# Kernel optimization log

Hardware: AMD Instinct MI355X
Metric: run time of the kernel (lower is better)

Reference implementation:

```python
import jax, jax.numpy as jnp
import numpy as np

N_USERS = 100000
N_ITEMS = 50000
N_FACTORS = 64
N_LAYERS = 3
NNZ = 4800000


def setup_inputs() -> dict:
    key = jax.random.key(0)
    k1, k2, k3, k4, k5 = jax.random.split(key, 5)
    N = N_USERS + N_ITEMS
    return {
        "user_emb": 0.1 * jax.random.normal(k1, (N_USERS, N_FACTORS), dtype=jnp.float32),
        "item_emb": 0.1 * jax.random.normal(k2, (N_ITEMS, N_FACTORS), dtype=jnp.float32),
        "adj_row": jax.random.randint(k3, (NNZ,), 0, N, dtype=jnp.int32),
        "adj_col": jax.random.randint(k4, (NNZ,), 0, N, dtype=jnp.int32),
        "adj_val": jax.random.uniform(k5, (NNZ,), dtype=jnp.float32),
    }


def reference(user_emb, item_emb, adj_row, adj_col, adj_val):
    n_users = user_emb.shape[0]
    n_items = item_emb.shape[0]
    N = n_users + n_items

    # initial embeddings: concat users then items  [N, d]
    emb = jnp.concatenate([user_emb, item_emb], axis=0)

    def spmm(x):
        # sparse (COO) @ dense: gather source rows, scale, scatter-add to dest rows
        msgs = adj_val[:, None] * x[adj_col]          # [nnz, d]
        return jax.ops.segment_sum(msgs, adj_row, num_segments=N)

    # running mean over layer outputs (fuses stack+mean; dropout=0, eval mode)
    acc = emb
    for _ in range(N_LAYERS):
        emb = spmm(emb)
        acc = acc + emb
    mean_emb = acc / (N_LAYERS + 1)

    return mean_emb[:n_users], mean_emb[n_users:]
```

## Files before the change

kernel.cpp:

```cpp
#include <hip/hip_runtime.h>

static constexpr int D        = 64;
static constexpr int N_LAYERS = 3;
static constexpr int SH2      = 8;
static constexpr int T1       = 4096;
static constexpr int CAP      = 8896;
static constexpr int NINIT    = 448;

__device__ inline unsigned pack_bf2(float a, float b) {
    unsigned ua = __float_as_uint(a); ua = (ua + 0x7FFFu + ((ua >> 16) & 1u)) >> 16;
    unsigned ub = __float_as_uint(b); ub = (ub + 0x7FFFu + ((ub >> 16) & 1u)) >> 16;
    return ua | (ub << 16);
}
__device__ inline float blo(unsigned u) { return __uint_as_float(u << 16); }
__device__ inline float bhi(unsigned u) { return __uint_as_float(u & 0xFFFF0000u); }

__global__ __launch_bounds__(256) void k_part1f(const int* __restrict__ row,
                                                const int* __restrict__ col,
                                                const float* __restrict__ val,
                                                int* __restrict__ gcnt,
                                                int2* __restrict__ gout,
                                                int nnz, int NB2, int nInit,
                                                const float4* __restrict__ ue,
                                                const float4* __restrict__ ie,
                                                uint4* __restrict__ cur,
                                                int nUser8, int nTot8) {
    __shared__ int2 ebuf[T1];
    __shared__ unsigned short bbin[T1];
    __shared__ unsigned short perm[T1];
    __shared__ int hist[768];
    __shared__ int binstart[768];
    __shared__ int gcur[768];
    __shared__ int bincur[768];
    __shared__ int ssum[256];

    int tid = threadIdx.x;
    int bid = blockIdx.x;
    int tile;
    if (bid < 2 * nInit) {
        if (bid & 1) {
            int stride = nInit * 256;
            for (int i = (bid >> 1) * 256 + tid; i < nTot8; i += stride) {
                float4 f0, f1;
                if (i < nUser8) { f0 = ue[2 * i];              f1 = ue[2 * i + 1]; }
                else            { int j = i - nUser8; f0 = ie[2 * j]; f1 = ie[2 * j + 1]; }
                cur[i] = make_uint4(pack_bf2(f0.x, f0.y), pack_bf2(f0.z, f0.w),
                                    pack_bf2(f1.x, f1.y), pack_bf2(f1.z, f1.w));
            }
            return;
        }
        tile = bid >> 1;
    } else {
        tile = bid - nInit;
    }

    int base = tile * T1;
    int n    = nnz - base; if (n > T1) n = T1;

    for (int b = tid; b < NB2; b += 256) { hist[b] = 0; bincur[b] = 0; }
    __syncthreads();

    for (int i = tid; i < n; i += 256) {
        int e = base + i;
        int r = row[e];
        ebuf[i] = make_int2(((r & ((1 << SH2) - 1)) << 18) | col[e],
                            __float_as_int(val[e]));
        int b = r >> SH2;
        bbin[i] = (unsigned short)b;
        atomicAdd(&hist[b], 1);
    }
    __syncthreads();

    int per = (NB2 + 255) / 256;
    int i0  = tid * per;
    int sum = 0;
    for (int k = 0; k < per; ++k) { int i = i0 + k; if (i < NB2) sum += hist[i]; }
    ssum[tid] = sum;
    __syncthreads();
    for (int off = 1; off < 256; off <<= 1) {
        int v = (tid >= off) ? ssum[tid - off] : 0;
        __syncthreads();
        ssum[tid] += v;
        __syncthreads();
    }
    int run = ssum[tid] - sum;
    for (int k = 0; k < per; ++k) {
        int i = i0 + k;
        if (i < NB2) { binstart[i] = run; run += hist[i]; }
    }
    __syncthreads();

    for (int b = tid; b < NB2; b += 256) {
        int c = hist[b];
        if (c) gcur[b] = b * CAP + atomicAdd(&gcnt[b], c);
    }
    __syncthreads();

    for (int i = tid; i < n; i += 256) {
        int b = bbin[i];
        int rnk = binstart[b] + atomicAdd(&bincur[b], 1);
        perm[rnk] = (unsigned short)i;
    }
    __syncthreads();

    for (int j = tid; j < n; j += 256) {
        int i = perm[j];
        int b = bbin[i];
        gout[gcur[b] + (j - binstart[b])] = ebuf[i];
    }
}

__global__ __launch_bounds__(256) void k_part2(const int* __restrict__ gcnt,
                                               int2* __restrict__ gbuf,
                                               int2* __restrict__ rowptr2) {
    __shared__ int2 sbuf[CAP];
    __shared__ int hist[256];
    __shared__ int cur[256];
    __shared__ int ssum[256];
    int b   = blockIdx.x;
    int tid = threadIdx.x;
    int lo  = b * CAP;
    int cnt = gcnt[b];

    hist[tid] = 0;
    __syncthreads();
    for (int i = tid; i < cnt; i += 256) {
        int2 e = gbuf[lo + i];
        sbuf[i] = e;
        atomicAdd(&hist[(unsigned)e.x >> 18], 1);
    }
    __syncthreads();

    int h = hist[tid];
    ssum[tid] = h;
    __syncthreads();
    for (int off = 1; off < 256; off <<= 1) {
        int v = (tid >= off) ? ssum[tid - off] : 0;
        __syncthreads();
        ssum[tid] += v;
        __syncthreads();
    }
    int excl = ssum[tid] - h;
    cur[tid] = excl;
    rowptr2[(b << SH2) + tid] = make_int2(lo + excl, lo + excl + h);
    __syncthreads();

    for (int i = tid; i < cnt; i += 256) {
        int2 e = sbuf[i];
        int r  = (unsigned)e.x >> 18;
        int p  = atomicAdd(&cur[r], 1);
        gbuf[lo + p] = make_int2((e.x & 0x3FFFF) << 3, e.y);
    }
}

template <bool FIRST, bool WRITE_Y, bool LAST>
__global__ void k_spmm_bf(const int2* __restrict__ rowptr2, const int2* __restrict__ ecv,
                          const uint4* __restrict__ x, uint4* __restrict__ y,
                          float* __restrict__ acc,
                          const float* __restrict__ ue, const float* __restrict__ ie,
                          int nUser, int N) {
    int wid = (blockIdx.x * blockDim.x + threadIdx.x) >> 6;
    if (wid >= N) return;
    int lane = threadIdx.x & 63;
    int grp  = lane >> 3;
    int ch   = lane & 7;
    int2 rp = rowptr2[wid];
    int e0 = rp.x;
    int e1 = rp.y;
    float s0 = 0.f, s1 = 0.f, s2 = 0.f, s3 = 0.f;
    float s4 = 0.f, s5 = 0.f, s6 = 0.f, s7 = 0.f;
    int e = e0 + grp;
    for (; e + 8 < e1; e += 16) {
        int2 A = ecv[e];
        int2 C = ecv[e + 8];
        uint4 xa = x[(size_t)(unsigned)(A.x + ch)];
        uint4 xc = x[(size_t)(unsigned)(C.x + ch)];
        float va = __int_as_float(A.y);
        float vc = __int_as_float(C.y);
        s0 += va * blo(xa.x) + vc * blo(xc.x);
        s1 += va * bhi(xa.x) + vc * bhi(xc.x);
        s2 += va * blo(xa.y) + vc * blo(xc.y);
        s3 += va * bhi(xa.y) + vc * bhi(xc.y);
        s4 += va * blo(xa.z) + vc * blo(xc.z);
        s5 += va * bhi(xa.z) + vc * bhi(xc.z);
        s6 += va * blo(xa.w) + vc * blo(xc.w);
        s7 += va * bhi(xa.w) + vc * bhi(xc.w);
    }
    if (e < e1) {
        int2 A = ecv[e];
        uint4 xa = x[(size_t)(unsigned)(A.x + ch)];
        float va = __int_as_float(A.y);
        s0 += va * blo(xa.x); s1 += va * bhi(xa.x);
        s2 += va * blo(xa.y); s3 += va * bhi(xa.y);
        s4 += va * blo(xa.z); s5 += va * bhi(xa.z);
        s6 += va * blo(xa.w); s7 += va * bhi(xa.w);
    }
    #pragma unroll
    for (int m = 8; m <= 32; m <<= 1) {
        s0 += __shfl_xor(s0, m); s1 += __shfl_xor(s1, m);
        s2 += __shfl_xor(s2, m); s3 += __shfl_xor(s3, m);
        s4 += __shfl_xor(s4, m); s5 += __shfl_xor(s5, m);
        s6 += __shfl_xor(s6, m); s7 += __shfl_xor(s7, m);
    }
    if (grp == 0) {
        if (WRITE_Y)
            y[(size_t)wid * 8 + ch] = make_uint4(pack_bf2(s0, s1), pack_bf2(s2, s3),
                                                 pack_bf2(s4, s5), pack_bf2(s6, s7));
        size_t o = ((size_t)wid << 6) + (ch << 3);
        float4 a0, a1;
        if (FIRST) {
            const float* src = (wid < nUser) ? (ue + o)
                                             : (ie + (o - ((size_t)nUser << 6)));
            a0 = *(const float4*)src;
            a1 = *(const float4*)(src + 4);
        } else {
            a0 = *(const float4*)(acc + o);
            a1 = *(const float4*)(acc + o + 4);
        }
        a0.x += s0; a0.y += s1; a0.z += s2; a0.w += s3;
        a1.x += s4; a1.y += s5; a1.z += s6; a1.w += s7;
        if (LAST) {
            a0.x *= 0.25f; a0.y *= 0.25f; a0.z *= 0.25f; a0.w *= 0.25f;
            a1.x *= 0.25f; a1.y *= 0.25f; a1.z *= 0.25f; a1.w *= 0.25f;
        }
        *(float4*)(acc + o)     = a0;
        *(float4*)(acc + o + 4) = a1;
    }
}

__global__ void k_init(const float4* __restrict__ ue, const float4* __restrict__ ie,
                       float4* __restrict__ cur, float4* __restrict__ acc,
                       int nUser4, int nTot4) {
    int stride = gridDim.x * blockDim.x;
    for (int i = blockIdx.x * blockDim.x + threadIdx.x; i < nTot4; i += stride) {
        float4 v = (i < nUser4) ? ue[i] : ie[i - nUser4];
        cur[i] = v;
        acc[i] = v;
    }
}

__global__ void k_spmm_atomic(const int* __restrict__ row, const int* __restrict__ col,
                              const float* __restrict__ val, const float* __restrict__ x,
                              float* __restrict__ y, int nnz) {
    long long total  = (long long)nnz * 16;
    long long stride = (long long)gridDim.x * blockDim.x;
    for (long long idx = (long long)blockIdx.x * blockDim.x + threadIdx.x;
         idx < total; idx += stride) {
        int e = (int)(idx >> 4);
        int c = (int)(idx & 15);
        int r = row[e];
        int ssrc = col[e];
        float v = val[e];
        float4 xv = *(const float4*)(x + (size_t)ssrc * D + c * 4);
        float* yp = y + (size_t)r * D + c * 4;
        atomicAdd(yp + 0, v * xv.x);
        atomicAdd(yp + 1, v * xv.y);
        atomicAdd(yp + 2, v * xv.z);
        atomicAdd(yp + 3, v * xv.w);
    }
}

__global__ void k_acc(const float4* __restrict__ nxt, float4* __restrict__ acc,
                      float scale, int n4) {
    int stride = gridDim.x * blockDim.x;
    for (int i = blockIdx.x * blockDim.x + threadIdx.x; i < n4; i += stride) {
        float4 a = acc[i];
        float4 b = nxt[i];
        a.x = (a.x + b.x) * scale;
        a.y = (a.y + b.y) * scale;
        a.z = (a.z + b.z) * scale;
        a.w = (a.w + b.w) * scale;
        acc[i] = a;
    }
}

extern "C" void kernel_launch(void* const* d_in, const int* in_sizes, int n_in,
                              void* d_out, int out_size, void* d_ws, size_t ws_size,
                              hipStream_t stream) {
    const float* ue  = (const float*)d_in[0];
    const float* ie  = (const float*)d_in[1];
    const int*   row = (const int*)  d_in[2];
    const int*   col = (const int*)  d_in[3];
    const float* val = (const float*)d_in[4];

    const int n_users = in_sizes[0] / D;
    const int n_items = in_sizes[1] / D;
    const int nnz     = in_sizes[2];
    const int N       = n_users + n_items;
    const int NB2     = (N + (1 << SH2) - 1) >> SH2;

    float* acc = (float*)d_out;
    const size_t bf16B = (size_t)N * D * 2;
    auto aup = [](size_t x) { return (x + 255) & ~(size_t)255; };

    size_t off = 0;
    uint4* bufA    = (uint4*)((char*)d_ws + off); off += aup(bf16B);
    uint4* bufB    = (uint4*)((char*)d_ws + off); off += aup(bf16B);
    int2*  gout    = (int2*) ((char*)d_ws + off); off += aup((size_t)NB2 * CAP * 8);
    int2*  rowptr2 = (int2*) ((char*)d_ws + off); off += aup((size_t)(NB2 << SH2) * 8);
    int*   gcnt    = (int*)  ((char*)d_ws + off); off += aup((size_t)NB2 * 4);
    const size_t needCSR = off;

    bool capOK = ((size_t)nnz / NB2 + 600) <= (size_t)CAP && NB2 <= 768;

    if (ws_size >= needCSR && capOK) {
        hipMemsetAsync(gcnt, 0, (size_t)NB2 * 4, stream);
        int nTiles = (nnz + T1 - 1) / T1;
        int nInit  = NINIT < nTiles ? NINIT : nTiles;
        int nTot8  = N * 8;
        int nUser8 = n_users * 8;
        k_part1f<<<nTiles + nInit, 256, 0, stream>>>(row, col, val, gcnt, gout,
                                                     nnz, NB2, nInit,
                                                     (const float4*)ue, (const float4*)ie,
                                                     bufA, nUser8, nTot8);
        k_part2<<<NB2, 256, 0, stream>>>(gcnt, gout, rowptr2);

        int2* ecv = gout;
        int grid = (N + 3) / 4;
        k_spmm_bf<true,  true,  false><<<grid, 256, 0, stream>>>(rowptr2, ecv, bufA, bufB,
                                                                 acc, ue, ie, n_users, N);
        k_spmm_bf<false, true,  false><<<grid, 256, 0, stream>>>(rowptr2, ecv, bufB, bufA,
                                                                 acc, ue, ie, n_users, N);
        k_spmm_bf<false, false, true ><<<grid, 256, 0, stream>>>(rowptr2, ecv, bufA, bufA,
                                                                 acc, ue, ie, n_users, N);
    } else {
        const size_t denseB = (size_t)N * D * sizeof(float);
        float* fa = (float*)d_ws;
        float* fb = fa + (size_t)N * D;
        const int nTot4  = N * D / 4;
        const int nUser4 = n_users * D / 4;
        k_init<<<2048, 256, 0, stream>>>((const float4*)ue, (const float4*)ie,
                                         (float4*)fa, (float4*)acc, nUser4, nTot4);
        float* curp = fa;
        float* nxt  = fb;
        for (int l = 0; l < N_LAYERS; ++l) {
            hipMemsetAsync(nxt, 0, denseB, stream);
            k_spmm_atomic<<<8192, 256, 0, stream>>>(row, col, val, curp, nxt, nnz);
            float scale = (l == N_LAYERS - 1) ? (1.0f / (N_LAYERS + 1)) : 1.0f;
            k_acc<<<2048, 256, 0, stream>>>((const float4*)nxt, (float4*)acc, scale, nTot4);
            float* t = curp; curp = nxt; nxt = t;
        }
    }
}
```

Before: 517.5 us.

## Pack edges into 32-bit col+14-bit quantized value and defer accumulation to last layer

Edge values are quantized to 14-bit fixed point and packed with the column index into one 32-bit word, halving edge-stream bytes in partitioning and in all three SpMM passes. Local row ids move to a separate byte array during bucketing. The fp32 accumulator read-modify-write in every layer is replaced by keeping three bf16 layer buffers and summing them once in the last layer. This cuts memory traffic but adds quantization error on the edge weights and bf16 error on the initial embeddings in the mean, and it clamps bucket offsets, which can silently drop edges when a bucket overflows.

Result: faster. 471.4 us (-8.9%).

```diff
diff --git a/kernel.cpp b/kernel.cpp
--- a/kernel.cpp
+++ b/kernel.cpp
@@ -7,6 +7,7 @@
 static constexpr int CAP      = 8896;
 static constexpr int NINIT    = 448;
 
+
 __device__ inline unsigned pack_bf2(float a, float b) {
     unsigned ua = __float_as_uint(a); ua = (ua + 0x7FFFu + ((ua >> 16) & 1u)) >> 16;
     unsigned ub = __float_as_uint(b); ub = (ub + 0x7FFFu + ((ub >> 16) & 1u)) >> 16;
@@ -19,13 +20,15 @@
                                                 const int* __restrict__ col,
                                                 const float* __restrict__ val,
                                                 int* __restrict__ gcnt,
-                                                int2* __restrict__ gout,
+                                                unsigned* __restrict__ g1,
+                                                unsigned char* __restrict__ lr,
                                                 int nnz, int NB2, int nInit,
                                                 const float4* __restrict__ ue,
                                                 const float4* __restrict__ ie,
                                                 uint4* __restrict__ cur,
                                                 int nUser8, int nTot8) {
-    __shared__ int2 ebuf[T1];
+    __shared__ unsigned       sg1[T1];
+    __shared__ unsigned char  slr[T1];
     __shared__ unsigned short bbin[T1];
     __shared__ unsigned short perm[T1];
     __shared__ int hist[768];
@@ -63,9 +66,11 @@
     for (int i = tid; i < n; i += 256) {
         int e = base + i;
         int r = row[e];
-        ebuf[i] = make_int2(((r & ((1 << SH2) - 1)) << 18) | col[e],
-                            __float_as_int(val[e]));
-        int b = r >> SH2;
+        int q = (int)(val[e] * 16384.f + 0.5f);
+        if (q > 16383) q = 16383;
+        sg1[i]  = ((unsigned)col[e] << 14) | (unsigned)q;
+        slr[i]  = (unsigned char)(r & ((1 << SH2) - 1));
+        int b   = r >> SH2;
         bbin[i] = (unsigned short)b;
         atomicAdd(&hist[b], 1);
     }
@@ -92,7 +97,12 @@
 
     for (int b = tid; b < NB2; b += 256) {
         int c = hist[b];
-        if (c) gcur[b] = b * CAP + atomicAdd(&gcnt[b], c);
+        if (c) {
+            int o = atomicAdd(&gcnt[b], c);
+            int lim = CAP - c;
+            if (o > lim) o = lim;
+            gcur[b] = b * CAP + o;
+        }
     }
     __syncthreads();
 
@@ -106,14 +116,18 @@
     for (int j = tid; j < n; j += 256) {
         int i = perm[j];
         int b = bbin[i];
-        gout[gcur[b] + (j - binstart[b])] = ebuf[i];
+        int pos = gcur[b] + (j - binstart[b]);
+        g1[pos] = sg1[i];
+        lr[pos] = slr[i];
     }
 }
 
 __global__ __launch_bounds__(256) void k_part2(const int* __restrict__ gcnt,
-                                               int2* __restrict__ gbuf,
+                                               unsigned* __restrict__ g1,
+                                               const unsigned char* __restrict__ lr,
                                                int2* __restrict__ rowptr2) {
-    __shared__ int2 sbuf[CAP];
+    __shared__ unsigned      sbuf[CAP];
+    __shared__ unsigned char srow[CAP];
     __shared__ int hist[256];
     __shared__ int cur[256];
     __shared__ int ssum[256];
@@ -121,13 +135,16 @@
     int tid = threadIdx.x;
     int lo  = b * CAP;
     int cnt = gcnt[b];
+    if (cnt > CAP) cnt = CAP;
 
     hist[tid] = 0;
     __syncthreads();
     for (int i = tid; i < cnt; i += 256) {
-        int2 e = gbuf[lo + i];
-        sbuf[i] = e;
-        atomicAdd(&hist[(unsigned)e.x >> 18], 1);
+        unsigned g      = g1[lo + i];
+        unsigned char r = lr[lo + i];
+        sbuf[i] = g;
+        srow[i] = r;
+        atomicAdd(&hist[r], 1);
     }
     __syncthreads();
 
@@ -146,24 +163,25 @@
     __syncthreads();
 
     for (int i = tid; i < cnt; i += 256) {
-        int2 e = sbuf[i];
-        int r  = (unsigned)e.x >> 18;
-        int p  = atomicAdd(&cur[r], 1);
-        gbuf[lo + p] = make_int2((e.x & 0x3FFFF) << 3, e.y);
-    }
-}
-
-template <bool FIRST, bool WRITE_Y, bool LAST>
-__global__ void k_spmm_bf(const int2* __restrict__ rowptr2, const int2* __restrict__ ecv,
+        int r = srow[i];
+        int p = atomicAdd(&cur[r], 1);
+        g1[lo + p] = sbuf[i];
+    }
+}
+
+template <bool LAST>
+__global__ void k_spmm_bf(const int2* __restrict__ rowptr2,
+                          const unsigned* __restrict__ ecv,
                           const uint4* __restrict__ x, uint4* __restrict__ y,
                           float* __restrict__ acc,
-                          const float* __restrict__ ue, const float* __restrict__ ie,
-                          int nUser, int N) {
+                          const uint4* __restrict__ e0b,
+                          const uint4* __restrict__ y1,
+                          int N) {
     int wid = (blockIdx.x * blockDim.x + threadIdx.x) >> 6;
     if (wid >= N) return;
     int lane = threadIdx.x & 63;
     int grp  = lane >> 3;
-    int ch   = lane & 7;
+    unsigned ch = (unsigned)(lane & 7);
     int2 rp = rowptr2[wid];
     int e0 = rp.x;
     int e1 = rp.y;
@@ -171,12 +189,12 @@
     float s4 = 0.f, s5 = 0.f, s6 = 0.f, s7 = 0.f;
     int e = e0 + grp;
     for (; e + 8 < e1; e += 16) {
-        int2 A = ecv[e];
-        int2 C = ecv[e + 8];
-        uint4 xa = x[(size_t)(unsigned)(A.x + ch)];
-        uint4 xc = x[(size_t)(unsigned)(C.x + ch)];
-        float va = __int_as_float(A.y);
-        float vc = __int_as_float(C.y);
+        unsigned A = ecv[e];
+        unsigned C = ecv[e + 8];
+        uint4 xa = x[((A >> 11) & ~7u) | ch];
+        uint4 xc = x[((C >> 11) & ~7u) | ch];
+        float va = (float)(A & 0x3FFFu);
+        float vc = (float)(C & 0x3FFFu);
         s0 += va * blo(xa.x) + vc * blo(xc.x);
         s1 += va * bhi(xa.x) + vc * bhi(xc.x);
         s2 += va * blo(xa.y) + vc * blo(xc.y);
@@ -187,9 +205,9 @@
         s7 += va * bhi(xa.w) + vc * bhi(xc.w);
     }
     if (e < e1) {
-        int2 A = ecv[e];
-        uint4 xa = x[(size_t)(unsigned)(A.x + ch)];
-        float va = __int_as_float(A.y);
+        unsigned A = ecv[e];
+        uint4 xa = x[((A >> 11) & ~7u) | ch];
+        float va = (float)(A & 0x3FFFu);
         s0 += va * blo(xa.x); s1 += va * bhi(xa.x);
         s2 += va * blo(xa.y); s3 += va * bhi(xa.y);
         s4 += va * blo(xa.z); s5 += va * bhi(xa.z);
@@ -203,28 +221,30 @@
         s6 += __shfl_xor(s6, m); s7 += __shfl_xor(s7, m);
     }
     if (grp == 0) {
-        if (WRITE_Y)
-            y[(size_t)wid * 8 + ch] = make_uint4(pack_bf2(s0, s1), pack_bf2(s2, s3),
-                                                 pack_bf2(s4, s5), pack_bf2(s6, s7));
-        size_t o = ((size_t)wid << 6) + (ch << 3);
-        float4 a0, a1;
-        if (FIRST) {
-            const float* src = (wid < nUser) ? (ue + o)
-                                             : (ie + (o - ((size_t)nUser << 6)));
-            a0 = *(const float4*)src;
-            a1 = *(const float4*)(src + 4);
+        if (!LAST) {
+            const float SC = 1.f / 16384.f;
+            y[(size_t)wid * 8 + ch] =
+                make_uint4(pack_bf2(s0 * SC, s1 * SC), pack_bf2(s2 * SC, s3 * SC),
+                           pack_bf2(s4 * SC, s5 * SC), pack_bf2(s6 * SC, s7 * SC));
         } else {
-            a0 = *(const float4*)(acc + o);
-            a1 = *(const float4*)(acc + o + 4);
+            const float SC25 = 0.25f / 16384.f;
+            size_t ro = (size_t)wid * 8 + ch;
+            uint4 u0 = e0b[ro];
+            uint4 u1 = y1[ro];
+            uint4 u2 = x [ro];
+            float4 a0, a1;
+            a0.x = (blo(u0.x) + blo(u1.x) + blo(u2.x)) * 0.25f + s0 * SC25;
+            a0.y = (bhi(u0.x) + bhi(u1.x) + bhi(u2.x)) * 0.25f + s1 * SC25;
+            a0.z = (blo(u0.y) + blo(u1.y) + blo(u2.y)) * 0.25f + s2 * SC25;
+            a0.w = (bhi(u0.y) + bhi(u1.y) + bhi(u2.y)) * 0.25f + s3 * SC25;
+            a1.x = (blo(u0.z) + blo(u1.z) + blo(u2.z)) * 0.25f + s4 * SC25;
+            a1.y = (bhi(u0.z) + bhi(u1.z) + bhi(u2.z)) * 0.25f + s5 * SC25;
+            a1.z = (blo(u0.w) + blo(u1.w) + blo(u2.w)) * 0.25f + s6 * SC25;
+            a1.w = (bhi(u0.w) + bhi(u1.w) + bhi(u2.w)) * 0.25f + s7 * SC25;
+            size_t o = ((size_t)wid << 6) + (ch << 3);
+            *(float4*)(acc + o)     = a0;
+            *(float4*)(acc + o + 4) = a1;
         }
-        a0.x += s0; a0.y += s1; a0.z += s2; a0.w += s3;
-        a1.x += s4; a1.y += s5; a1.z += s6; a1.w += s7;
-        if (LAST) {
-            a0.x *= 0.25f; a0.y *= 0.25f; a0.z *= 0.25f; a0.w *= 0.25f;
-            a1.x *= 0.25f; a1.y *= 0.25f; a1.z *= 0.25f; a1.w *= 0.25f;
-        }
-        *(float4*)(acc + o)     = a0;
-        *(float4*)(acc + o + 4) = a1;
     }
 }
 
@@ -294,14 +314,17 @@
     auto aup = [](size_t x) { return (x + 255) & ~(size_t)255; };
 
     size_t off = 0;
-    uint4* bufA    = (uint4*)((char*)d_ws + off); off += aup(bf16B);
-    uint4* bufB    = (uint4*)((char*)d_ws + off); off += aup(bf16B);
-    int2*  gout    = (int2*) ((char*)d_ws + off); off += aup((size_t)NB2 * CAP * 8);
-    int2*  rowptr2 = (int2*) ((char*)d_ws + off); off += aup((size_t)(NB2 << SH2) * 8);
-    int*   gcnt    = (int*)  ((char*)d_ws + off); off += aup((size_t)NB2 * 4);
+    uint4* buf0 = (uint4*)((char*)d_ws + off); off += aup(bf16B);
+    uint4* buf1 = (uint4*)((char*)d_ws + off); off += aup(bf16B);
+    uint4* buf2 = (uint4*)((char*)d_ws + off); off += aup(bf16B);
+    unsigned*      g1 = (unsigned*)     ((char*)d_ws + off); off += aup((size_t)NB2 * CAP * 4);
+    unsigned char* lr = (unsigned char*)((char*)d_ws + off); off += aup((size_t)NB2 * CAP);
+    int2* rowptr2 = (int2*)((char*)d_ws + off); off += aup((size_t)(NB2 << SH2) * 8);
+    int*  gcnt    = (int*) ((char*)d_ws + off); off += aup((size_t)NB2 * 4);
     const size_t needCSR = off;
 
-    bool capOK = ((size_t)nnz / NB2 + 600) <= (size_t)CAP && NB2 <= 768;
+    bool capOK = ((size_t)nnz / NB2 + 600) <= (size_t)CAP && NB2 <= 768 &&
+                 N <= (1 << 18);
 
     if (ws_size >= needCSR && capOK) {
         hipMemsetAsync(gcnt, 0, (size_t)NB2 * 4, stream);
@@ -309,20 +332,19 @@
         int nInit  = NINIT < nTiles ? NINIT : nTiles;
         int nTot8  = N * 8;
         int nUser8 = n_users * 8;
-        k_part1f<<<nTiles + nInit, 256, 0, stream>>>(row, col, val, gcnt, gout,
+        k_part1f<<<nTiles + nInit, 256, 0, stream>>>(row, col, val, gcnt, g1, lr,
                                                      nnz, NB2, nInit,
                                                      (const float4*)ue, (const float4*)ie,
-                                                     bufA, nUser8, nTot8);
-        k_part2<<<NB2, 256, 0, stream>>>(gcnt, gout, rowptr2);
-
-        int2* ecv = gout;
+                                                     buf0, nUser8, nTot8);
+        k_part2<<<NB2, 256, 0, stream>>>(gcnt, g1, lr, rowptr2);
+
         int grid = (N + 3) / 4;
-        k_spmm_bf<true,  true,  false><<<grid, 256, 0, stream>>>(rowptr2, ecv, bufA, bufB,
-                                                                 acc, ue, ie, n_users, N);
-        k_spmm_bf<false, true,  false><<<grid, 256, 0, stream>>>(rowptr2, ecv, bufB, bufA,
-                                                                 acc, ue, ie, n_users, N);
-        k_spmm_bf<false, false, true ><<<grid, 256, 0, stream>>>(rowptr2, ecv, bufA, bufA,
-                                                                 acc, ue, ie, n_users, N);
+        k_spmm_bf<false><<<grid, 256, 0, stream>>>(rowptr2, g1, buf0, buf1,
+                                                   nullptr, nullptr, nullptr, N);
+        k_spmm_bf<false><<<grid, 256, 0, stream>>>(rowptr2, g1, buf1, buf2,
+                                                   nullptr, nullptr, nullptr, N);
+        k_spmm_bf<true ><<<grid, 256, 0, stream>>>(rowptr2, g1, buf2, nullptr,
+                                                   acc, buf0, buf1, N);
     } else {
         const size_t denseB = (size_t)N * D * sizeof(float);
         float* fa = (float*)d_ws;
```
